# Optimization experiments

Measured on AMD Instinct MI355X. Metric: run time of the kernel, lower is better.

Reference implementation:

```python
import jax, jax.numpy as jnp
import numpy as np

ACTIVE_TASK = 0
K = 4  # top-k experts

def setup_inputs() -> dict:
    key = jax.random.key(0)
    k1, k2, k3, k4 = jax.random.split(key, 4)
    B, L, H, E, T = 16, 8192, 768, 16, 8
    x = jax.random.normal(k1, (B, L, H), jnp.float32)
    task_full = jax.random.normal(k2, (T, H), jnp.float32)
    gate_w = jax.random.normal(k3, (H, E), jnp.float32) * 0.02   # f_gate Linear weight (transposed)
    gate_b = jnp.zeros((E,), jnp.float32)                         # f_gate Linear bias
    expert_w = jax.random.normal(k4, (E, H, H), jnp.float32) * 0.02  # ParallelExperts weight [E, in, out]
    return {"x": x, "task_full": task_full, "gate_w": gate_w, "gate_b": gate_b, "expert_w": expert_w}

def reference(x, task_full, gate_w, gate_b, expert_w):
    T = task_full.shape[0]
    E = gate_w.shape[1]
    # f_gate = SiLU -> Linear
    logits = jax.nn.silu(task_full) @ gate_w + gate_b            # [T, E]
    probs = jax.nn.softmax(logits, axis=1)                       # [T, E]
    top_k_gates, top_k_indices = jax.lax.top_k(probs, K)         # [T, K]
    # probs_full_quantized: one-hot mask of selected experts per task
    probs_full_quantized = jnp.zeros((T, E), jnp.float32).at[
        jnp.arange(T)[:, None], top_k_indices].set(1.0)
    active_probs = probs[ACTIVE_TASK]                            # [E]
    gates = top_k_gates[ACTIVE_TASK]                             # [K]
    idx = top_k_indices[ACTIVE_TASK]                             # [K] int
    # compute_gating on a single task row: batch_index = arange(K)//K == 0 for all
    # slots, so every selected expert consumes a copy of x[0] (length rows each),
    # and index_add accumulates all K weighted expert outputs into out[0].
    h = jnp.einsum('ld,kdo->klo', x[0], expert_w[idx])           # grouped expert GEMM [K, L, H]
    out0 = jnp.einsum('k,klo->lo', gates, h)                     # gate-weighted combine [L, H]
    out = jnp.zeros_like(x).at[0].add(out0)                      # scatter-add at batch_index (all 0)
    return 1.0 + out, active_probs, probs_full_quantized
```

## Files before the change

### kernel.cpp

```cpp
#include <hip/hip_runtime.h>
#include <hip/hip_bf16.h>

typedef __attribute__((ext_vector_type(8))) short short8;
typedef __attribute__((ext_vector_type(4))) float f32x4;

#define H_DIM 768
#define E_EXP 16
#define T_TASK 8
#define KSEL 4
#define L_SEQ 8192
#define B_BATCH 16
#define EW_STRIDE (768*768)

#define CVT_BLOCKS 3072
#define FILL1_BLOCKS 1280
#define GEMM_BLOCKS 384
#define FILL3_BLOCKS 1152

__global__ __launch_bounds__(256) void k1_gating_cvt_fill(
    const float* __restrict__ task_full,
    const float* __restrict__ gate_w,
    const float* __restrict__ gate_b,
    float* __restrict__ out_tail,
    float* __restrict__ ws_gates,
    int*   __restrict__ ws_idx,
    const float4* __restrict__ x,
    uint4* __restrict__ xb,
    float4* __restrict__ fill_p, size_t fill_n4) {
  const int bid = blockIdx.x;
  const int tid = threadIdx.x;
  if (bid == 0) {
    __shared__ float silu_s[T_TASK * H_DIM];
    __shared__ float logits[T_TASK][E_EXP];
    for (int i = tid; i < T_TASK * H_DIM; i += 256) {
      float v = task_full[i];
      silu_s[i] = v / (1.f + expf(-v));
    }
    __syncthreads();
    if (tid < T_TASK * E_EXP) {
      const int t = tid >> 4, e = tid & 15;
      float a0 = 0.f, a1 = 0.f, a2 = 0.f, a3 = 0.f;
      const float* sl = &silu_s[t * H_DIM];
      for (int h = 0; h < H_DIM; h += 4) {
        a0 += sl[h]     * gate_w[(h)     * E_EXP + e];
        a1 += sl[h + 1] * gate_w[(h + 1) * E_EXP + e];
        a2 += sl[h + 2] * gate_w[(h + 2) * E_EXP + e];
        a3 += sl[h + 3] * gate_w[(h + 3) * E_EXP + e];
      }
      logits[t][e] = (a0 + a1) + (a2 + a3) + gate_b[e];
    }
    __syncthreads();
    if (tid < T_TASK) {
      const int t = tid;
      float p[E_EXP];
      float m = -1e30f;
      for (int e = 0; e < E_EXP; ++e) m = fmaxf(m, logits[t][e]);
      float s = 0.f;
      for (int e = 0; e < E_EXP; ++e) { p[e] = expf(logits[t][e] - m); s += p[e]; }
      const float inv = 1.f / s;
      for (int e = 0; e < E_EXP; ++e) p[e] *= inv;
      bool used[E_EXP];
      for (int e = 0; e < E_EXP; ++e) used[e] = false;
      float g[KSEL]; int sel[KSEL];
      for (int k = 0; k < KSEL; ++k) {
        float bv = -1.f; int bi = 0;
        for (int e = 0; e < E_EXP; ++e)
          if (!used[e] && p[e] > bv) { bv = p[e]; bi = e; }
        used[bi] = true; sel[k] = bi; g[k] = bv;
      }
      for (int e = 0; e < E_EXP; ++e)
        out_tail[E_EXP + t * E_EXP + e] = used[e] ? 1.f : 0.f;
      if (t == 0) {
        for (int e = 0; e < E_EXP; ++e) out_tail[e] = p[e];
        for (int k = 0; k < KSEL; ++k) { ws_gates[k] = g[k]; ws_idx[k] = sel[k]; }
      }
    }
  } else if (bid <= CVT_BLOCKS) {
    const int i = (bid - 1) * 256 + tid;
    const float4 a = x[2 * i];
    const float4 b = x[2 * i + 1];
    alignas(16) __hip_bfloat16 h[8];
    h[0] = __float2bfloat16(a.x); h[1] = __float2bfloat16(a.y);
    h[2] = __float2bfloat16(a.z); h[3] = __float2bfloat16(a.w);
    h[4] = __float2bfloat16(b.x); h[5] = __float2bfloat16(b.y);
    h[6] = __float2bfloat16(b.z); h[7] = __float2bfloat16(b.w);
    xb[i] = *(const uint4*)h;
  } else {
    const int fb = bid - 1 - CVT_BLOCKS;
    size_t i = (size_t)fb * 256 + tid;
    const size_t stride = (size_t)FILL1_BLOCKS * 256;
    const float4 one = make_float4(1.f, 1.f, 1.f, 1.f);
    for (; i < fill_n4; i += stride) fill_p[i] = one;
  }
}

__global__ void build_wct_kernel(const float* __restrict__ expert_w,
                                 const float* __restrict__ gates,
                                 const int* __restrict__ idx,
                                 __hip_bfloat16* __restrict__ wct) {
  __shared__ float tile[32][33];
  const int d0 = blockIdx.x * 32, o0 = blockIdx.y * 32;
  const float g0 = gates[0], g1 = gates[1], g2 = gates[2], g3 = gates[3];
  const size_t e0 = (size_t)idx[0] * EW_STRIDE;
  const size_t e1 = (size_t)idx[1] * EW_STRIDE;
  const size_t e2 = (size_t)idx[2] * EW_STRIDE;
  const size_t e3 = (size_t)idx[3] * EW_STRIDE;
  const int c = threadIdx.x & 31;
  const int r0 = threadIdx.x >> 5;
#pragma unroll
  for (int it = 0; it < 4; ++it) {
    const int rr = it * 8 + r0;
    const size_t off = (size_t)(d0 + rr) * H_DIM + o0 + c;
    tile[rr][c] = g0 * expert_w[e0 + off] + g1 * expert_w[e1 + off] +
                  g2 * expert_w[e2 + off] + g3 * expert_w[e3 + off];
  }
  __syncthreads();
#pragma unroll
  for (int it = 0; it < 4; ++it) {
    const int rr = it * 8 + r0;
    wct[(size_t)(o0 + rr) * H_DIM + d0 + c] = __float2bfloat16(tile[c][rr]);
  }
}

__device__ __forceinline__ void gload_lds16(const void* g, void* l) {
  __builtin_amdgcn_global_load_lds((const __attribute__((address_space(1))) void*)g,
                                   (__attribute__((address_space(3))) void*)l, 16, 0, 0);
}

__global__ __launch_bounds__(256) void k3_gemm_fill(
    const __hip_bfloat16* __restrict__ A,
    const __hip_bfloat16* __restrict__ Bt,
    float* __restrict__ C,
    float4* __restrict__ fill_p, size_t fill_n4) {
  const int bid = blockIdx.x;
  const int tid = threadIdx.x;
  if (bid < GEMM_BLOCKS) {
    __shared__ __hip_bfloat16 As[128 * 32];
    __shared__ __hip_bfloat16 Bs[128 * 32];
    const int m0 = (bid & 63) * 128;
    const int n0 = (bid >> 6) * 128;
    const int lane = tid & 63;
    const int w = tid >> 6;
    const int wr = w >> 1, wc = w & 1;
    const int r = tid >> 2, s = tid & 3;
    const __hip_bfloat16* ga = A  + (size_t)(m0 + r) * H_DIM + s * 8;
    const __hip_bfloat16* gb = Bt + (size_t)(n0 + r) * H_DIM + s * 8;
    f32x4 acc[4][4] = {};
    const int arow = wr * 64 + (lane & 15);
    const int brow = wc * 64 + (lane & 15);
    const int koff = (lane >> 4) * 8;
    for (int k0 = 0; k0 < H_DIM; k0 += 32) {
      gload_lds16(ga + k0,               &As[tid * 8]);
      gload_lds16(ga + 64 * H_DIM + k0,  &As[2048 + tid * 8]);
      gload_lds16(gb + k0,               &Bs[tid * 8]);
      gload_lds16(gb + 64 * H_DIM + k0,  &Bs[2048 + tid * 8]);
      __syncthreads();
      short8 av[4], bv[4];
#pragma unroll
      for (int i = 0; i < 4; ++i) av[i] = *(const short8*)&As[(arow + i * 16) * 32 + koff];
#pragma unroll
      for (int j = 0; j < 4; ++j) bv[j] = *(const short8*)&Bs[(brow + j * 16) * 32 + koff];
#pragma unroll
      for (int i = 0; i < 4; ++i)
#pragma unroll
        for (int j = 0; j < 4; ++j)
          acc[i][j] = __builtin_amdgcn_mfma_f32_16x16x32_bf16(av[i], bv[j], acc[i][j], 0, 0, 0);
      __syncthreads();
    }
    const int crow0 = m0 + wr * 64 + (lane >> 4) * 4;
    const int ccol0 = n0 + wc * 64 + (lane & 15);
#pragma unroll
    for (int i = 0; i < 4; ++i)
#pragma unroll
      for (int j = 0; j < 4; ++j)
#pragma unroll
        for (int q = 0; q < 4; ++q)
          C[(size_t)(crow0 + i * 16 + q) * H_DIM + ccol0 + j * 16] = 1.0f + acc[i][j][q];
  } else {
    const int fb = bid - GEMM_BLOCKS;
    size_t i = (size_t)fb * 256 + tid;
    const size_t stride = (size_t)FILL3_BLOCKS * 256;
    const float4 one = make_float4(1.f, 1.f, 1.f, 1.f);
    for (; i < fill_n4; i += stride) fill_p[i] = one;
  }
}

extern "C" void kernel_launch(void* const* d_in, const int* in_sizes, int n_in,
                              void* d_out, int out_size, void* d_ws, size_t ws_size,
                              hipStream_t stream) {
  const float* x         = (const float*)d_in[0];
  const float* task_full = (const float*)d_in[1];
  const float* gate_w    = (const float*)d_in[2];
  const float* gate_b    = (const float*)d_in[3];
  const float* expert_w  = (const float*)d_in[4];
  float* out = (float*)d_out;

  const size_t n_out_main = (size_t)B_BATCH * L_SEQ * H_DIM;
  float* out_tail = out + n_out_main;

  float* ws_gates = (float*)d_ws;
  int*   ws_idx   = (int*)((char*)d_ws + 16);
  __hip_bfloat16* wct = (__hip_bfloat16*)((char*)d_ws + 512);
  __hip_bfloat16* x0b = (__hip_bfloat16*)((char*)d_ws + 512 + (size_t)EW_STRIDE * 2);

  const size_t fill1_n4 = (size_t)8 * L_SEQ * H_DIM / 4;
  k1_gating_cvt_fill<<<1 + CVT_BLOCKS + FILL1_BLOCKS, 256, 0, stream>>>(
      task_full, gate_w, gate_b, out_tail, ws_gates, ws_idx,
      (const float4*)x, (uint4*)x0b,
      (float4*)(out + (size_t)1 * L_SEQ * H_DIM), fill1_n4);

  build_wct_kernel<<<dim3(24, 24), 256, 0, stream>>>(expert_w, ws_gates, ws_idx, wct);

  const size_t fill3_n4 = (size_t)7 * L_SEQ * H_DIM / 4;
  k3_gemm_fill<<<GEMM_BLOCKS + FILL3_BLOCKS, 256, 0, stream>>>(
      x0b, wct, out,
      (float4*)(out + (size_t)9 * L_SEQ * H_DIM), fill3_n4);
}
```

Baseline: 119.1 us.

## Fuse gating into weight-build blocks and convert x to bf16 inside GEMM

Each of the 576 weight-build blocks now recomputes the small gating (SiLU, logits, softmax, top-k) redundantly, so a separate kernel launch and the workspace round trip disappear. The standalone x-to-bf16 conversion pass is dropped. The GEMM instead loads fp32 x directly, converts it in registers and stores it to a padded LDS tile. This cuts the pipeline from three launches to two and removes a write-then-read of 12MB of bf16 x, at the cost of redundant gating work per block and synchronous fp32 A loads inside the GEMM loop. Fill block counts are rebalanced between the two kernels.

```diff
diff --git a/kernel.cpp b/kernel.cpp
--- a/kernel.cpp
+++ b/kernel.cpp
@@ -12,113 +12,113 @@
 #define B_BATCH 16
 #define EW_STRIDE (768*768)
 
-#define CVT_BLOCKS 3072
-#define FILL1_BLOCKS 1280
+#define WCT_BLOCKS 576
+#define FILLA_BLOCKS 1472
 #define GEMM_BLOCKS 384
-#define FILL3_BLOCKS 1152
-
-__global__ __launch_bounds__(256) void k1_gating_cvt_fill(
+#define FILLB_BLOCKS 1472
+#define AS_LD 40
+
+__device__ __forceinline__ void gating_block(
     const float* __restrict__ task_full,
     const float* __restrict__ gate_w,
     const float* __restrict__ gate_b,
+    float* silu_s, float (*logits)[E_EXP],
+    float* g_sh, int* i_sh,
+    float* __restrict__ out_tail, bool write_tail) {
+  const int tid = threadIdx.x;
+  for (int i = tid; i < T_TASK * H_DIM; i += 256) {
+    float v = task_full[i];
+    silu_s[i] = v / (1.f + expf(-v));
+  }
+  __syncthreads();
+  if (tid < T_TASK * E_EXP) {
+    const int t = tid >> 4, e = tid & 15;
+    float a0 = 0.f, a1 = 0.f, a2 = 0.f, a3 = 0.f;
+    const float* sl = &silu_s[t * H_DIM];
+    for (int h = 0; h < H_DIM; h += 4) {
+      a0 += sl[h]     * gate_w[(h)     * E_EXP + e];
+      a1 += sl[h + 1] * gate_w[(h + 1) * E_EXP + e];
+      a2 += sl[h + 2] * gate_w[(h + 2) * E_EXP + e];
+      a3 += sl[h + 3] * gate_w[(h + 3) * E_EXP + e];
+    }
+    logits[t][e] = (a0 + a1) + (a2 + a3) + gate_b[e];
+  }
+  __syncthreads();
+  if (tid < T_TASK) {
+    const int t = tid;
+    float p[E_EXP];
+    float m = -1e30f;
+    for (int e = 0; e < E_EXP; ++e) m = fmaxf(m, logits[t][e]);
+    float s = 0.f;
+    for (int e = 0; e < E_EXP; ++e) { p[e] = expf(logits[t][e] - m); s += p[e]; }
+    const float inv = 1.f / s;
+    for (int e = 0; e < E_EXP; ++e) p[e] *= inv;
+    bool used[E_EXP];
+    for (int e = 0; e < E_EXP; ++e) used[e] = false;
+    float g[KSEL]; int sel[KSEL];
+    for (int k = 0; k < KSEL; ++k) {
+      float bv = -1.f; int bi = 0;
+      for (int e = 0; e < E_EXP; ++e)
+        if (!used[e] && p[e] > bv) { bv = p[e]; bi = e; }
+      used[bi] = true; sel[k] = bi; g[k] = bv;
+    }
+    if (write_tail) {
+      for (int e = 0; e < E_EXP; ++e)
+        out_tail[E_EXP + t * E_EXP + e] = used[e] ? 1.f : 0.f;
+      if (t == 0)
+        for (int e = 0; e < E_EXP; ++e) out_tail[e] = p[e];
+    }
+    if (t == 0)
+      for (int k = 0; k < KSEL; ++k) { g_sh[k] = g[k]; i_sh[k] = sel[k]; }
+  }
+  __syncthreads();
+}
+
+__global__ __launch_bounds__(256) void kA_wct_fill(
+    const float* __restrict__ task_full,
+    const float* __restrict__ gate_w,
+    const float* __restrict__ gate_b,
+    const float* __restrict__ expert_w,
+    __hip_bfloat16* __restrict__ wct,
     float* __restrict__ out_tail,
-    float* __restrict__ ws_gates,
-    int*   __restrict__ ws_idx,
-    const float4* __restrict__ x,
-    uint4* __restrict__ xb,
     float4* __restrict__ fill_p, size_t fill_n4) {
   const int bid = blockIdx.x;
   const int tid = threadIdx.x;
-  if (bid == 0) {
+  if (bid < WCT_BLOCKS) {
     __shared__ float silu_s[T_TASK * H_DIM];
     __shared__ float logits[T_TASK][E_EXP];
-    for (int i = tid; i < T_TASK * H_DIM; i += 256) {
-      float v = task_full[i];
-      silu_s[i] = v / (1.f + expf(-v));
+    __shared__ float g_sh[KSEL];
+    __shared__ int   i_sh[KSEL];
+    __shared__ float tile[32][33];
+    gating_block(task_full, gate_w, gate_b, silu_s, logits, g_sh, i_sh,
+                 out_tail, bid == 0);
+    const float g0 = g_sh[0], g1 = g_sh[1], g2 = g_sh[2], g3 = g_sh[3];
+    const size_t e0 = (size_t)i_sh[0] * EW_STRIDE;
+    const size_t e1 = (size_t)i_sh[1] * EW_STRIDE;
+    const size_t e2 = (size_t)i_sh[2] * EW_STRIDE;
+    const size_t e3 = (size_t)i_sh[3] * EW_STRIDE;
+    const int d0 = (bid % 24) * 32, o0 = (bid / 24) * 32;
+    const int c = tid & 31;
+    const int r0 = tid >> 5;
+#pragma unroll
+    for (int it = 0; it < 4; ++it) {
+      const int rr = it * 8 + r0;
+      const size_t off = (size_t)(d0 + rr) * H_DIM + o0 + c;
+      tile[rr][c] = g0 * expert_w[e0 + off] + g1 * expert_w[e1 + off] +
+                    g2 * expert_w[e2 + off] + g3 * expert_w[e3 + off];
     }
     __syncthreads();
-    if (tid < T_TASK * E_EXP) {
-      const int t = tid >> 4, e = tid & 15;
-      float a0 = 0.f, a1 = 0.f, a2 = 0.f, a3 = 0.f;
-      const float* sl = &silu_s[t * H_DIM];
-      for (int h = 0; h < H_DIM; h += 4) {
-        a0 += sl[h]     * gate_w[(h)     * E_EXP + e];
-        a1 += sl[h + 1] * gate_w[(h + 1) * E_EXP + e];
-        a2 += sl[h + 2] * gate_w[(h + 2) * E_EXP + e];
-        a3 += sl[h + 3] * gate_w[(h + 3) * E_EXP + e];
-      }
-      logits[t][e] = (a0 + a1) + (a2 + a3) + gate_b[e];
-    }
-    __syncthreads();
-    if (tid < T_TASK) {
-      const int t = tid;
-      float p[E_EXP];
-      float m = -1e30f;
-      for (int e = 0; e < E_EXP; ++e) m = fmaxf(m, logits[t][e]);
-      float s = 0.f;
-      for (int e = 0; e < E_EXP; ++e) { p[e] = expf(logits[t][e] - m); s += p[e]; }
-      const float inv = 1.f / s;
-      for (int e = 0; e < E_EXP; ++e) p[e] *= inv;
-      bool used[E_EXP];
-      for (int e = 0; e < E_EXP; ++e) used[e] = false;
-      float g[KSEL]; int sel[KSEL];
-      for (int k = 0; k < KSEL; ++k) {
-        float bv = -1.f; int bi = 0;
-        for (int e = 0; e < E_EXP; ++e)
-          if (!used[e] && p[e] > bv) { bv = p[e]; bi = e; }
-        used[bi] = true; sel[k] = bi; g[k] = bv;
-      }
-      for (int e = 0; e < E_EXP; ++e)
-        out_tail[E_EXP + t * E_EXP + e] = used[e] ? 1.f : 0.f;
-      if (t == 0) {
-        for (int e = 0; e < E_EXP; ++e) out_tail[e] = p[e];
-        for (int k = 0; k < KSEL; ++k) { ws_gates[k] = g[k]; ws_idx[k] = sel[k]; }
-      }
-    }
-  } else if (bid <= CVT_BLOCKS) {
-    const int i = (bid - 1) * 256 + tid;
-    const float4 a = x[2 * i];
-    const float4 b = x[2 * i + 1];
-    alignas(16) __hip_bfloat16 h[8];
-    h[0] = __float2bfloat16(a.x); h[1] = __float2bfloat16(a.y);
-    h[2] = __float2bfloat16(a.z); h[3] = __float2bfloat16(a.w);
-    h[4] = __float2bfloat16(b.x); h[5] = __float2bfloat16(b.y);
-    h[6] = __float2bfloat16(b.z); h[7] = __float2bfloat16(b.w);
-    xb[i] = *(const uint4*)h;
+#pragma unroll
+    for (int it = 0; it < 4; ++it) {
+      const int rr = it * 8 + r0;
+      wct[(size_t)(o0 + rr) * H_DIM + d0 + c] = __float2bfloat16(tile[c][rr]);
+    }
   } else {
-    const int fb = bid - 1 - CVT_BLOCKS;
+    const int fb = bid - WCT_BLOCKS;
     size_t i = (size_t)fb * 256 + tid;
-    const size_t stride = (size_t)FILL1_BLOCKS * 256;
+    const size_t stride = (size_t)FILLA_BLOCKS * 256;
     const float4 one = make_float4(1.f, 1.f, 1.f, 1.f);
     for (; i < fill_n4; i += stride) fill_p[i] = one;
-  }
-}
-
-__global__ void build_wct_kernel(const float* __restrict__ expert_w,
-                                 const float* __restrict__ gates,
-                                 const int* __restrict__ idx,
-                                 __hip_bfloat16* __restrict__ wct) {
-  __shared__ float tile[32][33];
-  const int d0 = blockIdx.x * 32, o0 = blockIdx.y * 32;
-  const float g0 = gates[0], g1 = gates[1], g2 = gates[2], g3 = gates[3];
-  const size_t e0 = (size_t)idx[0] * EW_STRIDE;
-  const size_t e1 = (size_t)idx[1] * EW_STRIDE;
-  const size_t e2 = (size_t)idx[2] * EW_STRIDE;
-  const size_t e3 = (size_t)idx[3] * EW_STRIDE;
-  const int c = threadIdx.x & 31;
-  const int r0 = threadIdx.x >> 5;
-#pragma unroll
-  for (int it = 0; it < 4; ++it) {
-    const int rr = it * 8 + r0;
-    const size_t off = (size_t)(d0 + rr) * H_DIM + o0 + c;
-    tile[rr][c] = g0 * expert_w[e0 + off] + g1 * expert_w[e1 + off] +
-                  g2 * expert_w[e2 + off] + g3 * expert_w[e3 + off];
-  }
-  __syncthreads();
-#pragma unroll
-  for (int it = 0; it < 4; ++it) {
-    const int rr = it * 8 + r0;
-    wct[(size_t)(o0 + rr) * H_DIM + d0 + c] = __float2bfloat16(tile[c][rr]);
   }
 }
 
@@ -127,37 +127,51 @@
                                    (__attribute__((address_space(3))) void*)l, 16, 0, 0);
 }
 
-__global__ __launch_bounds__(256) void k3_gemm_fill(
-    const __hip_bfloat16* __restrict__ A,
+__global__ __launch_bounds__(256) void kB_gemm_fill(
+    const float* __restrict__ X,
     const __hip_bfloat16* __restrict__ Bt,
     float* __restrict__ C,
     float4* __restrict__ fill_p, size_t fill_n4) {
   const int bid = blockIdx.x;
   const int tid = threadIdx.x;
   if (bid < GEMM_BLOCKS) {
-    __shared__ __hip_bfloat16 As[128 * 32];
+    __shared__ __hip_bfloat16 As[128 * AS_LD];
     __shared__ __hip_bfloat16 Bs[128 * 32];
     const int m0 = (bid & 63) * 128;
     const int n0 = (bid >> 6) * 128;
     const int lane = tid & 63;
     const int w = tid >> 6;
     const int wr = w >> 1, wc = w & 1;
-    const int r = tid >> 2, s = tid & 3;
-    const __hip_bfloat16* ga = A  + (size_t)(m0 + r) * H_DIM + s * 8;
-    const __hip_bfloat16* gb = Bt + (size_t)(n0 + r) * H_DIM + s * 8;
+    const int ra = tid >> 1, sa = tid & 1;
+    const int rb = tid >> 2, sb = tid & 3;
+    const float* gx = X + (size_t)(m0 + ra) * H_DIM + sa * 16;
+    const __hip_bfloat16* gb = Bt + (size_t)(n0 + rb) * H_DIM + sb * 8;
     f32x4 acc[4][4] = {};
     const int arow = wr * 64 + (lane & 15);
     const int brow = wc * 64 + (lane & 15);
     const int koff = (lane >> 4) * 8;
     for (int k0 = 0; k0 < H_DIM; k0 += 32) {
-      gload_lds16(ga + k0,               &As[tid * 8]);
-      gload_lds16(ga + 64 * H_DIM + k0,  &As[2048 + tid * 8]);
-      gload_lds16(gb + k0,               &Bs[tid * 8]);
-      gload_lds16(gb + 64 * H_DIM + k0,  &Bs[2048 + tid * 8]);
+      gload_lds16(gb + k0,              &Bs[tid * 8]);
+      gload_lds16(gb + 64 * H_DIM + k0, &Bs[2048 + tid * 8]);
+      const float4 f0 = *(const float4*)(gx + k0);
+      const float4 f1 = *(const float4*)(gx + k0 + 4);
+      const float4 f2 = *(const float4*)(gx + k0 + 8);
+      const float4 f3 = *(const float4*)(gx + k0 + 12);
+      alignas(16) __hip_bfloat16 hb[16];
+      hb[0]  = __float2bfloat16(f0.x); hb[1]  = __float2bfloat16(f0.y);
+      hb[2]  = __float2bfloat16(f0.z); hb[3]  = __float2bfloat16(f0.w);
+      hb[4]  = __float2bfloat16(f1.x); hb[5]  = __float2bfloat16(f1.y);
+      hb[6]  = __float2bfloat16(f1.z); hb[7]  = __float2bfloat16(f1.w);
+      hb[8]  = __float2bfloat16(f2.x); hb[9]  = __float2bfloat16(f2.y);
+      hb[10] = __float2bfloat16(f2.z); hb[11] = __float2bfloat16(f2.w);
+      hb[12] = __float2bfloat16(f3.x); hb[13] = __float2bfloat16(f3.y);
+      hb[14] = __float2bfloat16(f3.z); hb[15] = __float2bfloat16(f3.w);
+      *(uint4*)&As[ra * AS_LD + sa * 16]     = *(const uint4*)&hb[0];
+      *(uint4*)&As[ra * AS_LD + sa * 16 + 8] = *(const uint4*)&hb[8];
       __syncthreads();
       short8 av[4], bv[4];
 #pragma unroll
-      for (int i = 0; i < 4; ++i) av[i] = *(const short8*)&As[(arow + i * 16) * 32 + koff];
+      for (int i = 0; i < 4; ++i) av[i] = *(const short8*)&As[(arow + i * 16) * AS_LD + koff];
 #pragma unroll
       for (int j = 0; j < 4; ++j) bv[j] = *(const short8*)&Bs[(brow + j * 16) * 32 + koff];
 #pragma unroll
@@ -179,7 +193,7 @@
   } else {
     const int fb = bid - GEMM_BLOCKS;
     size_t i = (size_t)fb * 256 + tid;
-    const size_t stride = (size_t)FILL3_BLOCKS * 256;
+    const size_t stride = (size_t)FILLB_BLOCKS * 256;
     const float4 one = make_float4(1.f, 1.f, 1.f, 1.f);
     for (; i < fill_n4; i += stride) fill_p[i] = one;
   }
@@ -198,21 +212,15 @@
   const size_t n_out_main = (size_t)B_BATCH * L_SEQ * H_DIM;
   float* out_tail = out + n_out_main;
 
-  float* ws_gates = (float*)d_ws;
-  int*   ws_idx   = (int*)((char*)d_ws + 16);
-  __hip_bfloat16* wct = (__hip_bfloat16*)((char*)d_ws + 512);
-  __hip_bfloat16* x0b = (__hip_bfloat16*)((char*)d_ws + 512 + (size_t)EW_STRIDE * 2);
-
-  const size_t fill1_n4 = (size_t)8 * L_SEQ * H_DIM / 4;
-  k1_gating_cvt_fill<<<1 + CVT_BLOCKS + FILL1_BLOCKS, 256, 0, stream>>>(
-      task_full, gate_w, gate_b, out_tail, ws_gates, ws_idx,
-      (const float4*)x, (uint4*)x0b,
-      (float4*)(out + (size_t)1 * L_SEQ * H_DIM), fill1_n4);
-
-  build_wct_kernel<<<dim3(24, 24), 256, 0, stream>>>(expert_w, ws_gates, ws_idx, wct);
-
-  const size_t fill3_n4 = (size_t)7 * L_SEQ * H_DIM / 4;
-  k3_gemm_fill<<<GEMM_BLOCKS + FILL3_BLOCKS, 256, 0, stream>>>(
-      x0b, wct, out,
-      (float4*)(out + (size_t)9 * L_SEQ * H_DIM), fill3_n4);
-}
+  __hip_bfloat16* wct = (__hip_bfloat16*)d_ws;
+
+  const size_t fillA_n4 = (size_t)8 * L_SEQ * H_DIM / 4;
+  kA_wct_fill<<<WCT_BLOCKS + FILLA_BLOCKS, 256, 0, stream>>>(
+      task_full, gate_w, gate_b, expert_w, wct, out_tail,
+      (float4*)(out + (size_t)1 * L_SEQ * H_DIM), fillA_n4);
+
+  const size_t fillB_n4 = (size_t)7 * L_SEQ * H_DIM / 4;
+  kB_gemm_fill<<<GEMM_BLOCKS + FILLB_BLOCKS, 256, 0, stream>>>(
+      x, wct, out,
+      (float4*)(out + (size_t)9 * L_SEQ * H_DIM), fillB_n4);
+}
```

Result: slower. 128.5 us (+7.9%).

## Fuse gating and weight-combine into first kernel, dropping a launch

Applied to the files above, without the earlier changes.

Each of the 576 weight-combine blocks now recomputes the gating softmax and top-k redundantly, then builds its tile of the gate-weighted bf16 transposed expert weight in the same launch as the x conversion and the fill. This removes the separate build_wct kernel and its launch and serialization gap. The cost is redundant gating work (SiLU over 8x768 and a small GEMV per block) and larger LDS use per block. It also reorders GEMM tile indexing so blocks sharing an M row are adjacent, and rebalances the fill block counts.

```diff
diff --git a/kernel.cpp b/kernel.cpp
--- a/kernel.cpp
+++ b/kernel.cpp
@@ -13,25 +13,40 @@
 #define EW_STRIDE (768*768)
 
 #define CVT_BLOCKS 3072
-#define FILL1_BLOCKS 1280
+#define WCT_BLOCKS 576
+#define FILL1_BLOCKS 1408
 #define GEMM_BLOCKS 384
-#define FILL3_BLOCKS 1152
-
-__global__ __launch_bounds__(256) void k1_gating_cvt_fill(
+#define FILL2_BLOCKS 1472
+
+__global__ __launch_bounds__(256) void k1_cvt_wct_fill(
+    const float4* __restrict__ x,
     const float* __restrict__ task_full,
     const float* __restrict__ gate_w,
     const float* __restrict__ gate_b,
+    const float* __restrict__ expert_w,
+    __hip_bfloat16* __restrict__ wct,
+    uint4* __restrict__ xb,
     float* __restrict__ out_tail,
-    float* __restrict__ ws_gates,
-    int*   __restrict__ ws_idx,
-    const float4* __restrict__ x,
-    uint4* __restrict__ xb,
     float4* __restrict__ fill_p, size_t fill_n4) {
   const int bid = blockIdx.x;
   const int tid = threadIdx.x;
-  if (bid == 0) {
+  if (bid < CVT_BLOCKS) {
+    const int i = bid * 256 + tid;
+    const float4 a = x[2 * i];
+    const float4 b = x[2 * i + 1];
+    alignas(16) __hip_bfloat16 h[8];
+    h[0] = __float2bfloat16(a.x); h[1] = __float2bfloat16(a.y);
+    h[2] = __float2bfloat16(a.z); h[3] = __float2bfloat16(a.w);
+    h[4] = __float2bfloat16(b.x); h[5] = __float2bfloat16(b.y);
+    h[6] = __float2bfloat16(b.z); h[7] = __float2bfloat16(b.w);
+    xb[i] = *(const uint4*)h;
+  } else if (bid < CVT_BLOCKS + WCT_BLOCKS) {
     __shared__ float silu_s[T_TASK * H_DIM];
     __shared__ float logits[T_TASK][E_EXP];
+    __shared__ float g_sh[KSEL];
+    __shared__ int   i_sh[KSEL];
+    __shared__ float tile[32][33];
+    const int wb = bid - CVT_BLOCKS;
     for (int i = tid; i < T_TASK * H_DIM; i += 256) {
       float v = task_full[i];
       silu_s[i] = v / (1.f + expf(-v));
@@ -68,25 +83,39 @@
           if (!used[e] && p[e] > bv) { bv = p[e]; bi = e; }
         used[bi] = true; sel[k] = bi; g[k] = bv;
       }
-      for (int e = 0; e < E_EXP; ++e)
-        out_tail[E_EXP + t * E_EXP + e] = used[e] ? 1.f : 0.f;
-      if (t == 0) {
-        for (int e = 0; e < E_EXP; ++e) out_tail[e] = p[e];
-        for (int k = 0; k < KSEL; ++k) { ws_gates[k] = g[k]; ws_idx[k] = sel[k]; }
+      if (wb == 0) {
+        for (int e = 0; e < E_EXP; ++e)
+          out_tail[E_EXP + t * E_EXP + e] = used[e] ? 1.f : 0.f;
+        if (t == 0)
+          for (int e = 0; e < E_EXP; ++e) out_tail[e] = p[e];
       }
-    }
-  } else if (bid <= CVT_BLOCKS) {
-    const int i = (bid - 1) * 256 + tid;
-    const float4 a = x[2 * i];
-    const float4 b = x[2 * i + 1];
-    alignas(16) __hip_bfloat16 h[8];
-    h[0] = __float2bfloat16(a.x); h[1] = __float2bfloat16(a.y);
-    h[2] = __float2bfloat16(a.z); h[3] = __float2bfloat16(a.w);
-    h[4] = __float2bfloat16(b.x); h[5] = __float2bfloat16(b.y);
-    h[6] = __float2bfloat16(b.z); h[7] = __float2bfloat16(b.w);
-    xb[i] = *(const uint4*)h;
+      if (t == 0)
+        for (int k = 0; k < KSEL; ++k) { g_sh[k] = g[k]; i_sh[k] = sel[k]; }
+    }
+    __syncthreads();
+    const float g0 = g_sh[0], g1 = g_sh[1], g2 = g_sh[2], g3 = g_sh[3];
+    const size_t e0 = (size_t)i_sh[0] * EW_STRIDE;
+    const size_t e1 = (size_t)i_sh[1] * EW_STRIDE;
+    const size_t e2 = (size_t)i_sh[2] * EW_STRIDE;
+    const size_t e3 = (size_t)i_sh[3] * EW_STRIDE;
+    const int d0 = (wb % 24) * 32, o0 = (wb / 24) * 32;
+    const int c = tid & 31;
+    const int r0 = tid >> 5;
+#pragma unroll
+    for (int it = 0; it < 4; ++it) {
+      const int rr = it * 8 + r0;
+      const size_t off = (size_t)(d0 + rr) * H_DIM + o0 + c;
+      tile[rr][c] = g0 * expert_w[e0 + off] + g1 * expert_w[e1 + off] +
+                    g2 * expert_w[e2 + off] + g3 * expert_w[e3 + off];
+    }
+    __syncthreads();
+#pragma unroll
+    for (int it = 0; it < 4; ++it) {
+      const int rr = it * 8 + r0;
+      wct[(size_t)(o0 + rr) * H_DIM + d0 + c] = __float2bfloat16(tile[c][rr]);
+    }
   } else {
-    const int fb = bid - 1 - CVT_BLOCKS;
+    const int fb = bid - CVT_BLOCKS - WCT_BLOCKS;
     size_t i = (size_t)fb * 256 + tid;
     const size_t stride = (size_t)FILL1_BLOCKS * 256;
     const float4 one = make_float4(1.f, 1.f, 1.f, 1.f);
@@ -94,40 +123,12 @@
   }
 }
 
-__global__ void build_wct_kernel(const float* __restrict__ expert_w,
-                                 const float* __restrict__ gates,
-                                 const int* __restrict__ idx,
-                                 __hip_bfloat16* __restrict__ wct) {
-  __shared__ float tile[32][33];
-  const int d0 = blockIdx.x * 32, o0 = blockIdx.y * 32;
-  const float g0 = gates[0], g1 = gates[1], g2 = gates[2], g3 = gates[3];
-  const size_t e0 = (size_t)idx[0] * EW_STRIDE;
-  const size_t e1 = (size_t)idx[1] * EW_STRIDE;
-  const size_t e2 = (size_t)idx[2] * EW_STRIDE;
-  const size_t e3 = (size_t)idx[3] * EW_STRIDE;
-  const int c = threadIdx.x & 31;
-  const int r0 = threadIdx.x >> 5;
-#pragma unroll
-  for (int it = 0; it < 4; ++it) {
-    const int rr = it * 8 + r0;
-    const size_t off = (size_t)(d0 + rr) * H_DIM + o0 + c;
-    tile[rr][c] = g0 * expert_w[e0 + off] + g1 * expert_w[e1 + off] +
-                  g2 * expert_w[e2 + off] + g3 * expert_w[e3 + off];
-  }
-  __syncthreads();
-#pragma unroll
-  for (int it = 0; it < 4; ++it) {
-    const int rr = it * 8 + r0;
-    wct[(size_t)(o0 + rr) * H_DIM + d0 + c] = __float2bfloat16(tile[c][rr]);
-  }
-}
-
 __device__ __forceinline__ void gload_lds16(const void* g, void* l) {
   __builtin_amdgcn_global_load_lds((const __attribute__((address_space(1))) void*)g,
                                    (__attribute__((address_space(3))) void*)l, 16, 0, 0);
 }
 
-__global__ __launch_bounds__(256) void k3_gemm_fill(
+__global__ __launch_bounds__(256) void k2_gemm_fill(
     const __hip_bfloat16* __restrict__ A,
     const __hip_bfloat16* __restrict__ Bt,
     float* __restrict__ C,
@@ -137,8 +138,8 @@
   if (bid < GEMM_BLOCKS) {
     __shared__ __hip_bfloat16 As[128 * 32];
     __shared__ __hip_bfloat16 Bs[128 * 32];
-    const int m0 = (bid & 63) * 128;
-    const int n0 = (bid >> 6) * 128;
+    const int m0 = (bid / 6) * 128;
+    const int n0 = (bid % 6) * 128;
     const int lane = tid & 63;
     const int w = tid >> 6;
     const int wr = w >> 1, wc = w & 1;
@@ -179,7 +180,7 @@
   } else {
     const int fb = bid - GEMM_BLOCKS;
     size_t i = (size_t)fb * 256 + tid;
-    const size_t stride = (size_t)FILL3_BLOCKS * 256;
+    const size_t stride = (size_t)FILL2_BLOCKS * 256;
     const float4 one = make_float4(1.f, 1.f, 1.f, 1.f);
     for (; i < fill_n4; i += stride) fill_p[i] = one;
   }
@@ -198,21 +199,17 @@
   const size_t n_out_main = (size_t)B_BATCH * L_SEQ * H_DIM;
   float* out_tail = out + n_out_main;
 
-  float* ws_gates = (float*)d_ws;
-  int*   ws_idx   = (int*)((char*)d_ws + 16);
-  __hip_bfloat16* wct = (__hip_bfloat16*)((char*)d_ws + 512);
-  __hip_bfloat16* x0b = (__hip_bfloat16*)((char*)d_ws + 512 + (size_t)EW_STRIDE * 2);
+  __hip_bfloat16* wct = (__hip_bfloat16*)d_ws;
+  __hip_bfloat16* x0b = (__hip_bfloat16*)((char*)d_ws + (size_t)EW_STRIDE * 2);
 
   const size_t fill1_n4 = (size_t)8 * L_SEQ * H_DIM / 4;
-  k1_gating_cvt_fill<<<1 + CVT_BLOCKS + FILL1_BLOCKS, 256, 0, stream>>>(
-      task_full, gate_w, gate_b, out_tail, ws_gates, ws_idx,
-      (const float4*)x, (uint4*)x0b,
+  k1_cvt_wct_fill<<<CVT_BLOCKS + WCT_BLOCKS + FILL1_BLOCKS, 256, 0, stream>>>(
+      (const float4*)x, task_full, gate_w, gate_b, expert_w,
+      wct, (uint4*)x0b, out_tail,
       (float4*)(out + (size_t)1 * L_SEQ * H_DIM), fill1_n4);
 
-  build_wct_kernel<<<dim3(24, 24), 256, 0, stream>>>(expert_w, ws_gates, ws_idx, wct);
-
-  const size_t fill3_n4 = (size_t)7 * L_SEQ * H_DIM / 4;
-  k3_gemm_fill<<<GEMM_BLOCKS + FILL3_BLOCKS, 256, 0, stream>>>(
+  const size_t fill2_n4 = (size_t)7 * L_SEQ * H_DIM / 4;
+  k2_gemm_fill<<<GEMM_BLOCKS + FILL2_BLOCKS, 256, 0, stream>>>(
       x0b, wct, out,
-      (float4*)(out + (size_t)9 * L_SEQ * H_DIM), fill3_n4);
-}
+      (float4*)(out + (size_t)9 * L_SEQ * H_DIM), fill2_n4);
+}
```

After: 119.3 us. About the same (+0.2%).
